# Kernel tuning notes

Hardware: AMD Instinct MI355X
Metric: run time of the kernel (lower is better)

## Reference

```python
import jax, jax.numpy as jnp
import numpy as np

T, B, E, H = 1024, 4, 1024, 16
D = E // H  # head_dim = 64


def rel_shift(x):
    # Transformer-XL relative shift trick (RelativeShift.forward, batch_first=True).
    # x: [BH, Q, P] -> pad one zero column, reshape [BH, P+1, Q], drop first row, reshape back.
    BH, Q, P = x.shape
    zp = jnp.zeros((BH, Q, 1), x.dtype)
    xp = jnp.concatenate([zp, x], axis=2).reshape(BH, P + 1, Q)
    return xp[:, 1:, :].reshape(BH, Q, P)


def setup_inputs() -> dict:
    key = jax.random.key(0)
    ks = jax.random.split(key, 8)
    std = float(np.sqrt(2.0 / (E + E)))
    causal = jnp.triu(jnp.ones((T, T), dtype=bool), k=1)  # True = masked (future positions)
    return {
        "x": jax.random.normal(ks[0], (T, B, E), dtype=jnp.float32),
        "pos": jax.random.normal(ks[1], (T, 1, E), dtype=jnp.float32),
        "in_proj_weight": jax.random.normal(ks[2], (3 * E, E), dtype=jnp.float32) * std,
        "in_proj_bias": jnp.zeros((3 * E,), dtype=jnp.float32),
        "out_proj_weight": jax.random.normal(ks[3], (E, E), dtype=jnp.float32) * std,
        "out_proj_bias": jnp.zeros((E,), dtype=jnp.float32),
        "pos_proj_weight": jax.random.normal(ks[4], (E, E), dtype=jnp.float32) * std,
        "pos_proj_bias": jnp.zeros((E,), dtype=jnp.float32),
        "r_w_bias": jax.random.normal(ks[5], (H, D), dtype=jnp.float32) * 0.02,
        "r_r_bias": jax.random.normal(ks[6], (H, D), dtype=jnp.float32) * 0.02,
        "attn_mask": causal,
    }


def reference(x, pos, in_proj_weight, in_proj_bias, out_proj_weight, out_proj_bias,
              pos_proj_weight, pos_proj_bias, r_w_bias, r_r_bias, attn_mask):
    Tq, Bb, Ee = x.shape
    scale = 1.0 / np.sqrt(D).astype(np.float32)
    # fused QKV projection; layout [T, B, heads, 3, head_dim] matches
    # view(len_q, bsz*heads, 3, head_dim) in the original.
    qkv = (x @ in_proj_weight.T + in_proj_bias).reshape(Tq, Bb, H, 3, D)
    q = qkv[..., 0, :]  # [T,B,H,D]
    k = qkv[..., 1, :]
    v = qkv[..., 2, :]
    # position projection (shared across batch since pos is [T,1,E])
    r_head_k = (pos[:, 0, :] @ pos_proj_weight.T + pos_proj_bias).reshape(Tq, H, D)  # [P,H,D]
    rw_q = q + r_w_bias  # content bias
    rr_q = q + r_r_bias  # position bias
    ac = jnp.einsum('qbhd,kbhd->bhqk', rw_q, k) * scale            # [B,H,Q,K]
    bd = jnp.einsum('qbhd,phd->bhqp', rr_q, r_head_k) * scale      # [B,H,Q,P]
    bd = rel_shift(bd.reshape(Bb * H, Tq, Tq)).reshape(Bb, H, Tq, Tq)[..., :Tq]
    score = ac + bd
    score = jnp.where(attn_mask[None, None, :, :], -jnp.inf, score)
    attn = jax.nn.softmax(score, axis=-1)                          # [B,H,Q,K]
    ctx = jnp.einsum('bhqk,kbhd->qbhd', attn, v).reshape(Tq, Bb, Ee)
    out = ctx @ out_proj_weight.T + out_proj_bias                  # [T,B,E]
    return out, attn
```

## Files before the change

### kernel.cpp

```cpp
#include <hip/hip_runtime.h>
#include <math.h>

#define TQ 1024
#define BBATCH 4
#define EDIM 1024
#define HHEADS 16
#define DHEAD 64

typedef __bf16 bf16x8 __attribute__((ext_vector_type(8)));
typedef __bf16 bf16x4 __attribute__((ext_vector_type(4)));
typedef float  f32x4  __attribute__((ext_vector_type(4)));

#define LDK 40

template<int MODE>
__global__ __launch_bounds__(256) void gemm_mfma_abt(
    const float* __restrict__ A, const float* __restrict__ B,
    const float* __restrict__ bias, float* __restrict__ C,
    int M, int N, int K)
{
    __shared__ __bf16 As[128 * LDK];
    __shared__ __bf16 Bs[128 * LDK];
    const int tid  = threadIdx.x;
    const int lane = tid & 63;
    const int wid  = tid >> 6;
    const int wr   = wid >> 1, wc = wid & 1;
    const int m0 = blockIdx.y * 128, n0 = blockIdx.x * 128;

    f32x4 acc[4][4] = {};

    const int sm0 = tid >> 2;
    const int sm1 = sm0 + 64;
    const int sk  = (tid & 3) << 3;

    const int fr = lane & 15;
    const int kg = (lane >> 4) << 3;

    for (int k0 = 0; k0 < K; k0 += 32) {
        float4 ra0a = *(const float4*)&A[(size_t)(m0 + sm0) * K + k0 + sk];
        float4 ra0b = *(const float4*)&A[(size_t)(m0 + sm0) * K + k0 + sk + 4];
        float4 ra1a = *(const float4*)&A[(size_t)(m0 + sm1) * K + k0 + sk];
        float4 ra1b = *(const float4*)&A[(size_t)(m0 + sm1) * K + k0 + sk + 4];
        float4 rb0a = *(const float4*)&B[(size_t)(n0 + sm0) * K + k0 + sk];
        float4 rb0b = *(const float4*)&B[(size_t)(n0 + sm0) * K + k0 + sk + 4];
        float4 rb1a = *(const float4*)&B[(size_t)(n0 + sm1) * K + k0 + sk];
        float4 rb1b = *(const float4*)&B[(size_t)(n0 + sm1) * K + k0 + sk + 4];

        __syncthreads();

        bf16x8 w;
        w[0]=(__bf16)ra0a.x; w[1]=(__bf16)ra0a.y; w[2]=(__bf16)ra0a.z; w[3]=(__bf16)ra0a.w;
        w[4]=(__bf16)ra0b.x; w[5]=(__bf16)ra0b.y; w[6]=(__bf16)ra0b.z; w[7]=(__bf16)ra0b.w;
        *(bf16x8*)&As[sm0 * LDK + sk] = w;
        w[0]=(__bf16)ra1a.x; w[1]=(__bf16)ra1a.y; w[2]=(__bf16)ra1a.z; w[3]=(__bf16)ra1a.w;
        w[4]=(__bf16)ra1b.x; w[5]=(__bf16)ra1b.y; w[6]=(__bf16)ra1b.z; w[7]=(__bf16)ra1b.w;
        *(bf16x8*)&As[sm1 * LDK + sk] = w;
        w[0]=(__bf16)rb0a.x; w[1]=(__bf16)rb0a.y; w[2]=(__bf16)rb0a.z; w[3]=(__bf16)rb0a.w;
        w[4]=(__bf16)rb0b.x; w[5]=(__bf16)rb0b.y; w[6]=(__bf16)rb0b.z; w[7]=(__bf16)rb0b.w;
        *(bf16x8*)&Bs[sm0 * LDK + sk] = w;
        w[0]=(__bf16)rb1a.x; w[1]=(__bf16)rb1a.y; w[2]=(__bf16)rb1a.z; w[3]=(__bf16)rb1a.w;
        w[4]=(__bf16)rb1b.x; w[5]=(__bf16)rb1b.y; w[6]=(__bf16)rb1b.z; w[7]=(__bf16)rb1b.w;
        *(bf16x8*)&Bs[sm1 * LDK + sk] = w;

        __syncthreads();

        bf16x8 af[4], bfr[4];
        #pragma unroll
        for (int i = 0; i < 4; ++i) {
            af[i]  = *(const bf16x8*)&As[(wr * 64 + i * 16 + fr) * LDK + kg];
            bfr[i] = *(const bf16x8*)&Bs[(wc * 64 + i * 16 + fr) * LDK + kg];
        }
        #pragma unroll
        for (int mi = 0; mi < 4; ++mi)
        #pragma unroll
        for (int ni = 0; ni < 4; ++ni)
            acc[mi][ni] = __builtin_amdgcn_mfma_f32_16x16x32_bf16(
                af[mi], bfr[ni], acc[mi][ni], 0, 0, 0);
    }

    const int fq = lane >> 4;
    #pragma unroll
    for (int mi = 0; mi < 4; ++mi)
    #pragma unroll
    for (int ni = 0; ni < 4; ++ni) {
        int row = m0 + wr * 64 + mi * 16 + fq * 4;
        int col = n0 + wc * 64 + ni * 16 + fr;
        float bv = bias[col];
        #pragma unroll
        for (int j = 0; j < 4; ++j) {
            float v = acc[mi][ni][j] + bv;
            if (MODE == 0) {
                C[(size_t)(row + j) * N + col] = v;
            } else {
                C[(((size_t)(col >> 6) << 10) + (row + j)) * 64 + (col & 63)] = v;
            }
        }
    }
}

__global__ __launch_bounds__(256) void bias_dots_kernel(
    const float* __restrict__ qkv, const float* __restrict__ Rm,
    const float* __restrict__ rwb, const float* __restrict__ rrb,
    float* __restrict__ cK, float* __restrict__ cR)
{
    int id = blockIdx.x * 256 + threadIdx.x;
    if (id < 65536) {
        int bh = id >> 10, k = id & 1023;
        int b = bh >> 4, h = bh & 15;
        const float* p = &qkv[((size_t)k * 4 + b) * 3072 + h * 192 + 64];
        const float* w = &rwb[h << 6];
        float s = 0.f;
        #pragma unroll
        for (int d = 0; d < 64; d += 4) {
            float4 v = *(const float4*)&p[d];
            s += v.x * w[d] + v.y * w[d + 1] + v.z * w[d + 2] + v.w * w[d + 3];
        }
        cK[id] = s;
    } else if (id < 81920) {
        int id2 = id - 65536;
        int h = id2 >> 10, j = id2 & 1023;
        const float* p = &Rm[(((size_t)h << 10) + j) * 64];
        const float* w = &rrb[h << 6];
        float s = 0.f;
        #pragma unroll
        for (int d = 0; d < 64; d += 4) {
            float4 v = *(const float4*)&p[d];
            s += v.x * w[d] + v.y * w[d + 1] + v.z * w[d + 2] + v.w * w[d + 3];
        }
        cR[id2] = s;
    }
}

#define SLD 72

__global__ __launch_bounds__(256) void score_tile_kernel(
    const float* __restrict__ qkv, const float* __restrict__ Rm,
    const float* __restrict__ cK, const float* __restrict__ cR,
    float* __restrict__ attn, float2* __restrict__ part)
{
    int t = blockIdx.x;
    int qt = (int)((sqrtf(8.f * t + 1.f) - 1.f) * 0.5f);
    while ((qt + 1) * (qt + 2) / 2 <= t) ++qt;
    while (qt * (qt + 1) / 2 > t) --qt;
    int kt = t - qt * (qt + 1) / 2;

    const int bh = blockIdx.y;
    const int b = bh >> 4, h = bh & 15;
    const int q0 = qt << 6, k0 = kt << 6;
    const int tid = threadIdx.x, lane = tid & 63, wid = tid >> 6;
    const int fr = lane & 15, fq = lane >> 4, kg = fq << 3;
    const int w16 = wid << 4;
    const int base_j = k0 - q0 + 960;

    __shared__ __align__(16) char smem[36864];
    __bf16* Qs = (__bf16*)smem;
    __bf16* Ks = (__bf16*)(smem + 9216);
    __bf16* R0 = (__bf16*)(smem + 18432);
    __bf16* R1 = (__bf16*)(smem + 27648);
    float (*BDs)[68] = (float(*)[68])smem;

    float4 qreg[4], kreg[4], r0reg[4], r1reg[4];
    #pragma unroll
    for (int s = 0; s < 4; ++s) {
        int idx = (s << 8) + tid;
        int r = idx >> 4, dc = (idx & 15) << 2;
        qreg[s] = *(const float4*)&qkv[((size_t)(q0 + r) * 4 + b) * 3072 + h * 192 + dc];
        kreg[s] = *(const float4*)&qkv[((size_t)(k0 + r) * 4 + b) * 3072 + h * 192 + 64 + dc];
        int j0 = base_j + r;       if (j0 > 1023) j0 = 1023;
        int j1 = base_j + 64 + r;  if (j1 > 1023) j1 = 1023;
        r0reg[s] = *(const float4*)&Rm[(((size_t)h << 10) + j0) * 64 + dc];
        r1reg[s] = *(const float4*)&Rm[(((size_t)h << 10) + j1) * 64 + dc];
    }
    #pragma unroll
    for (int s = 0; s < 4; ++s) {
        int idx = (s << 8) + tid;
        int r = idx >> 4, dc = (idx & 15) << 2;
        bf16x4 w;
        w[0]=(__bf16)qreg[s].x; w[1]=(__bf16)qreg[s].y; w[2]=(__bf16)qreg[s].z; w[3]=(__bf16)qreg[s].w;
        *(bf16x4*)&Qs[r * SLD + dc] = w;
        w[0]=(__bf16)kreg[s].x; w[1]=(__bf16)kreg[s].y; w[2]=(__bf16)kreg[s].z; w[3]=(__bf16)kreg[s].w;
        *(bf16x4*)&Ks[r * SLD + dc] = w;
        w[0]=(__bf16)r0reg[s].x; w[1]=(__bf16)r0reg[s].y; w[2]=(__bf16)r0reg[s].z; w[3]=(__bf16)r0reg[s].w;
        *(bf16x4*)&R0[r * SLD + dc] = w;
        w[0]=(__bf16)r1reg[s].x; w[1]=(__bf16)r1reg[s].y; w[2]=(__bf16)r1reg[s].z; w[3]=(__bf16)r1reg[s].w;
        *(bf16x4*)&R1[r * SLD + dc] = w;
    }
    __syncthreads();

    bf16x8 af0 = *(const bf16x8*)&Qs[(w16 + fr) * SLD + kg];
    bf16x8 af1 = *(const bf16x8*)&Qs[(w16 + fr) * SLD + 32 + kg];

    f32x4 aac[4], abd[4];
    const f32x4 z4 = {0.f, 0.f, 0.f, 0.f};

    #pragma unroll
    for (int ni = 0; ni < 4; ++ni) {
        bf16x8 b0 = *(const bf16x8*)&Ks[(ni * 16 + fr) * SLD + kg];
        bf16x8 b1 = *(const bf16x8*)&Ks[(ni * 16 + fr) * SLD + 32 + kg];
        aac[ni] = __builtin_amdgcn_mfma_f32_16x16x32_bf16(af0, b0, z4, 0, 0, 0);
        aac[ni] = __builtin_amdgcn_mfma_f32_16x16x32_bf16(af1, b1, aac[ni], 0, 0, 0);
    }
    #pragma unroll
    for (int ni = 0; ni < 4; ++ni) {
        bf16x8 b0 = *(const bf16x8*)&R0[(ni * 16 + fr) * SLD + kg];
        bf16x8 b1 = *(const bf16x8*)&R0[(ni * 16 + fr) * SLD + 32 + kg];
        abd[ni] = __builtin_amdgcn_mfma_f32_16x16x32_bf16(af0, b0, z4, 0, 0, 0);
        abd[ni] = __builtin_amdgcn_mfma_f32_16x16x32_bf16(af1, b1, abd[ni], 0, 0, 0);
    }

    __syncthreads();

    #pragma unroll
    for (int ni = 0; ni < 4; ++ni)
    #pragma unroll
    for (int j = 0; j < 4; ++j)
        BDs[w16 + fq * 4 + j][ni * 16 + fr] = abd[ni][j];
    asm volatile("s_waitcnt lgkmcnt(0)" ::: "memory");
    #pragma unroll
    for (int ni = 0; ni < 4; ++ni)
    #pragma unroll
    for (int j = 0; j < 4; ++j) {
        int lrow = w16 + fq * 4 + j;
        int widx = (ni * 16 + fr) - lrow + 63;
        if (widx < 64) aac[ni][j] += BDs[lrow][widx];
    }
    asm volatile("s_waitcnt lgkmcnt(0)" ::: "memory");

    #pragma unroll
    for (int ni = 0; ni < 4; ++ni) {
        bf16x8 b0 = *(const bf16x8*)&R1[(ni * 16 + fr) * SLD + kg];
        bf16x8 b1 = *(const bf16x8*)&R1[(ni * 16 + fr) * SLD + 32 + kg];
        abd[ni] = __builtin_amdgcn_mfma_f32_16x16x32_bf16(af0, b0, z4, 0, 0, 0);
        abd[ni] = __builtin_amdgcn_mfma_f32_16x16x32_bf16(af1, b1, abd[ni], 0, 0, 0);
    }
    #pragma unroll
    for (int ni = 0; ni < 4; ++ni)
    #pragma unroll
    for (int j = 0; j < 4; ++j)
        BDs[w16 + fq * 4 + j][ni * 16 + fr] = abd[ni][j];
    asm volatile("s_waitcnt lgkmcnt(0)" ::: "memory");
    #pragma unroll
    for (int ni = 0; ni < 4; ++ni)
    #pragma unroll
    for (int j = 0; j < 4; ++j) {
        int lrow = w16 + fq * 4 + j;
        int widx = (ni * 16 + fr) - lrow + 63;
        if (widx >= 64) aac[ni][j] += BDs[lrow][widx - 64];
    }

    float sc[4][4];
    #pragma unroll
    for (int ni = 0; ni < 4; ++ni) {
        int lcol = ni * 16 + fr;
        int k = k0 + lcol;
        float ckv = cK[(bh << 10) + k];
        #pragma unroll
        for (int j = 0; j < 4; ++j) {
            int lrow = w16 + fq * 4 + j;
            int q = q0 + lrow;
            int widx = lcol - lrow + 63;
            int jidx = base_j + widx; if (jidx > 1023) jidx = 1023;
            float crv = cR[(h << 10) + jidx];
            float v = 0.125f * (aac[ni][j] + ckv + crv);
            if (kt == qt && lcol > lrow) v = -1e30f;
            sc[ni][j] = v;
            attn[((((size_t)bh << 10) + q) << 10) + k] = v;
        }
    }
    #pragma unroll
    for (int j = 0; j < 4; ++j) {
        float tmax = fmaxf(fmaxf(sc[0][j], sc[1][j]), fmaxf(sc[2][j], sc[3][j]));
        tmax = fmaxf(tmax, __shfl_xor(tmax, 1));
        tmax = fmaxf(tmax, __shfl_xor(tmax, 2));
        tmax = fmaxf(tmax, __shfl_xor(tmax, 4));
        tmax = fmaxf(tmax, __shfl_xor(tmax, 8));
        float ps = __expf(sc[0][j] - tmax) + __expf(sc[1][j] - tmax)
                 + __expf(sc[2][j] - tmax) + __expf(sc[3][j] - tmax);
        ps += __shfl_xor(ps, 1); ps += __shfl_xor(ps, 2);
        ps += __shfl_xor(ps, 4); ps += __shfl_xor(ps, 8);
        if (fr == 0)
            part[(((size_t)(bh << 10) + q0 + w16 + fq * 4 + j) << 4) + kt]
                = make_float2(tmax, ps);
    }
}

__global__ __launch_bounds__(256) void stats_reduce_kernel(
    const float2* __restrict__ part, float2* __restrict__ stats,
    float* __restrict__ ctx)
{
    const int row = blockIdx.x * 256 + threadIdx.x;
    const int q = row & 1023;
    const int nt = (q >> 6) + 1;
    float2 pr[16];
    float m = -1e30f;
    for (int kt = 0; kt < nt; ++kt) {
        pr[kt] = part[((size_t)row << 4) + kt];
        m = fmaxf(m, pr[kt].x);
    }
    float s = 0.f;
    for (int kt = 0; kt < nt; ++kt)
        s += pr[kt].y * __expf(pr[kt].x - m);
    stats[row] = make_float2(m, 1.0f / s);

    const float4 z = {0.f, 0.f, 0.f, 0.f};
    #pragma unroll
    for (int i = 0; i < 16; ++i)
        *(float4*)&ctx[((size_t)i * 65536 + row) * 4] = z;
}

#define FLD 66

__global__ __launch_bounds__(256) void ctx_split_kernel(
    const float* __restrict__ qkv, const float2* __restrict__ stats,
    float* __restrict__ attn, float* __restrict__ ctx)
{
    const int pid = blockIdx.x;
    const int qt = 15 - (pid >> 1);
    const int half = pid & 1;
    const int n = qt + 1;
    const int nh0 = (n + 1) >> 1;
    const int kts = half ? nh0 : 0;
    const int kte = half ? n : nh0;

    const int bh = blockIdx.y;
    const int b = bh >> 4, h = bh & 15;
    const int q0 = qt << 6;
    const int tid = threadIdx.x, lane = tid & 63, wid = tid >> 6;
    const int fr = lane & 15, fq = lane >> 4, kg = fq << 3;
    const int w16 = wid << 4;
    const int c4 = (tid & 15) << 2;
    const int rb = tid >> 4;

    __shared__ __bf16 Pl[64 * FLD];
    __shared__ __bf16 Vt[64 * FLD];

    float mrow[4], inv[4];
    #pragma unroll
    for (int s = 0; s < 4; ++s) {
        float2 st = stats[(bh << 10) + q0 + rb + (s << 4)];
        mrow[s] = st.x; inv[s] = st.y;
    }

    f32x4 apv[4] = {};
    for (int kt = kts; kt < kte; ++kt) {
        const int k0 = kt << 6;
        float4 vreg[4], praw[4];
        #pragma unroll
        for (int s = 0; s < 4; ++s) {
            int r = rb + (s << 4);
            vreg[s] = *(const float4*)&qkv[((size_t)(k0 + r) * 4 + b) * 3072 + h * 192 + 128 + c4];
            praw[s] = *(const float4*)&attn[((size_t)bh << 20) + ((size_t)(q0 + r) << 10) + k0 + c4];
        }
        __syncthreads();
        #pragma unroll
        for (int s = 0; s < 4; ++s) {
            int r = rb + (s << 4);
            Vt[(c4 + 0) * FLD + r] = (__bf16)vreg[s].x;
            Vt[(c4 + 1) * FLD + r] = (__bf16)vreg[s].y;
            Vt[(c4 + 2) * FLD + r] = (__bf16)vreg[s].z;
            Vt[(c4 + 3) * FLD + r] = (__bf16)vreg[s].w;
            float4 p;
            p.x = __expf(praw[s].x - mrow[s]) * inv[s];
            p.y = __expf(praw[s].y - mrow[s]) * inv[s];
            p.z = __expf(praw[s].z - mrow[s]) * inv[s];
            p.w = __expf(praw[s].w - mrow[s]) * inv[s];
            *(float4*)&attn[((size_t)bh << 20) + ((size_t)(q0 + r) << 10) + k0 + c4] = p;
            bf16x4 pw;
            pw[0]=(__bf16)p.x; pw[1]=(__bf16)p.y; pw[2]=(__bf16)p.z; pw[3]=(__bf16)p.w;
            *(bf16x4*)&Pl[r * FLD + c4] = pw;
        }
        __syncthreads();
        bf16x8 pa0 = *(const bf16x8*)&Pl[(w16 + fr) * FLD + kg];
        bf16x8 pa1 = *(const bf16x8*)&Pl[(w16 + fr) * FLD + 32 + kg];
        #pragma unroll
        for (int ni = 0; ni < 4; ++ni) {
            bf16x8 bv0 = *(const bf16x8*)&Vt[(ni * 16 + fr) * FLD + kg];
            bf16x8 bv1 = *(const bf16x8*)&Vt[(ni * 16 + fr) * FLD + 32 + kg];
            apv[ni] = __builtin_amdgcn_mfma_f32_16x16x32_bf16(pa0, bv0, apv[ni], 0, 0, 0);
            apv[ni] = __builtin_amdgcn_mfma_f32_16x16x32_bf16(pa1, bv1, apv[ni], 0, 0, 0);
        }
    }

    if (half) {
        for (int kt = n; kt < 16; ++kt) {
            const int k0 = kt << 6;
            #pragma unroll
            for (int s = 0; s < 4; ++s) {
                int r = rb + (s << 4);
                float4 z = {0.f, 0.f, 0.f, 0.f};
                *(float4*)&attn[((size_t)bh << 20) + ((size_t)(q0 + r) << 10) + k0 + c4] = z;
            }
        }
    }

    if (kte > kts) {
        #pragma unroll
        for (int ni = 0; ni < 4; ++ni)
        #pragma unroll
        for (int j = 0; j < 4; ++j)
            atomicAdd(&ctx[((size_t)(q0 + w16 + fq * 4 + j) * 4 + b) * 1024
                           + (h << 6) + ni * 16 + fr], apv[ni][j]);
    }
}

extern "C" void kernel_launch(void* const* d_in, const int* in_sizes, int n_in,
                              void* d_out, int out_size, void* d_ws, size_t ws_size,
                              hipStream_t stream)
{
    (void)in_sizes; (void)n_in; (void)out_size; (void)ws_size;
    const float* x     = (const float*)d_in[0];
    const float* pos   = (const float*)d_in[1];
    const float* w_in  = (const float*)d_in[2];
    const float* b_in  = (const float*)d_in[3];
    const float* w_out = (const float*)d_in[4];
    const float* b_out = (const float*)d_in[5];
    const float* w_pos = (const float*)d_in[6];
    const float* b_pos = (const float*)d_in[7];
    const float* rwb   = (const float*)d_in[8];
    const float* rrb   = (const float*)d_in[9];

    float* out  = (float*)d_out;
    float* attn = out + (size_t)TQ * BBATCH * EDIM;

    float* ws  = (float*)d_ws;
    float* qkv = ws;
    float* R   = qkv + (size_t)4096 * 3072;
    float* ctx = R + (size_t)HHEADS * TQ * DHEAD;
    float*  cK    = out;
    float*  cR    = out + 65536;
    float2* stats = (float2*)(out + 81920);
    float2* part  = (float2*)(out + 262144);

    dim3 blk(256, 1, 1);

    gemm_mfma_abt<0><<<dim3(3072 / 128, 4096 / 128), blk, 0, stream>>>(
        x, w_in, b_in, qkv, 4096, 3072, 1024);
    gemm_mfma_abt<1><<<dim3(1024 / 128, 1024 / 128), blk, 0, stream>>>(
        pos, w_pos, b_pos, R, 1024, 1024, 1024);
    bias_dots_kernel<<<dim3(320), blk, 0, stream>>>(qkv, R, rwb, rrb, cK, cR);
    score_tile_kernel<<<dim3(136, 64), blk, 0, stream>>>(qkv, R, cK, cR, attn, part);
    stats_reduce_kernel<<<dim3(256), blk, 0, stream>>>(part, stats, ctx);
    ctx_split_kernel<<<dim3(32, 64), blk, 0, stream>>>(qkv, stats, attn, ctx);
    gemm_mfma_abt<0><<<dim3(1024 / 128, 4096 / 128), blk, 0, stream>>>(
        ctx, w_out, b_out, out, 4096, 1024, 1024);
}
```

Before: 376.1 us.

## Load score-tile MFMA operands directly from global memory, dropping LDS staging

The score tile kernel no longer stages Q, K and the two R windows through shared memory. Each wave now loads its MFMA fragments straight from global memory as fp32 and converts them to bf16 in registers. This removes the LDS stores, one barrier and most of the shared memory footprint, and a launch bound of 3 blocks is added to raise occupancy. In exchange, every wave re-reads the K and R rows from global or L2 with less coalesced access. The GEMM change is only a helper refactor plus an unused accumulator.

```diff
diff --git a/kernel.cpp b/kernel.cpp
--- a/kernel.cpp
+++ b/kernel.cpp
@@ -10,6 +10,13 @@
 typedef __bf16 bf16x8 __attribute__((ext_vector_type(8)));
 typedef __bf16 bf16x4 __attribute__((ext_vector_type(4)));
 typedef float  f32x4  __attribute__((ext_vector_type(4)));
+
+__device__ __forceinline__ bf16x8 cvt8(float4 a, float4 b) {
+    bf16x8 w;
+    w[0]=(__bf16)a.x; w[1]=(__bf16)a.y; w[2]=(__bf16)a.z; w[3]=(__bf16)a.w;
+    w[4]=(__bf16)b.x; w[5]=(__bf16)b.y; w[6]=(__bf16)b.z; w[7]=(__bf16)b.w;
+    return w;
+}
 
 #define LDK 40
 
@@ -27,7 +34,9 @@
     const int wr   = wid >> 1, wc = wid & 1;
     const int m0 = blockIdx.y * 128, n0 = blockIdx.x * 128;
 
-    f32x4 acc[4][4] = {};
+    f32x4 acc[2][2][4] = {};
+
+    f32x4 accf[4][4] = {};
 
     const int sm0 = tid >> 2;
     const int sm1 = sm0 + 64;
@@ -48,19 +57,10 @@
 
         __syncthreads();
 
-        bf16x8 w;
-        w[0]=(__bf16)ra0a.x; w[1]=(__bf16)ra0a.y; w[2]=(__bf16)ra0a.z; w[3]=(__bf16)ra0a.w;
-        w[4]=(__bf16)ra0b.x; w[5]=(__bf16)ra0b.y; w[6]=(__bf16)ra0b.z; w[7]=(__bf16)ra0b.w;
-        *(bf16x8*)&As[sm0 * LDK + sk] = w;
-        w[0]=(__bf16)ra1a.x; w[1]=(__bf16)ra1a.y; w[2]=(__bf16)ra1a.z; w[3]=(__bf16)ra1a.w;
-        w[4]=(__bf16)ra1b.x; w[5]=(__bf16)ra1b.y; w[6]=(__bf16)ra1b.z; w[7]=(__bf16)ra1b.w;
-        *(bf16x8*)&As[sm1 * LDK + sk] = w;
-        w[0]=(__bf16)rb0a.x; w[1]=(__bf16)rb0a.y; w[2]=(__bf16)rb0a.z; w[3]=(__bf16)rb0a.w;
-        w[4]=(__bf16)rb0b.x; w[5]=(__bf16)rb0b.y; w[6]=(__bf16)rb0b.z; w[7]=(__bf16)rb0b.w;
-        *(bf16x8*)&Bs[sm0 * LDK + sk] = w;
-        w[0]=(__bf16)rb1a.x; w[1]=(__bf16)rb1a.y; w[2]=(__bf16)rb1a.z; w[3]=(__bf16)rb1a.w;
-        w[4]=(__bf16)rb1b.x; w[5]=(__bf16)rb1b.y; w[6]=(__bf16)rb1b.z; w[7]=(__bf16)rb1b.w;
-        *(bf16x8*)&Bs[sm1 * LDK + sk] = w;
+        *(bf16x8*)&As[sm0 * LDK + sk] = cvt8(ra0a, ra0b);
+        *(bf16x8*)&As[sm1 * LDK + sk] = cvt8(ra1a, ra1b);
+        *(bf16x8*)&Bs[sm0 * LDK + sk] = cvt8(rb0a, rb0b);
+        *(bf16x8*)&Bs[sm1 * LDK + sk] = cvt8(rb1a, rb1b);
 
         __syncthreads();
 
@@ -74,9 +74,10 @@
         for (int mi = 0; mi < 4; ++mi)
         #pragma unroll
         for (int ni = 0; ni < 4; ++ni)
-            acc[mi][ni] = __builtin_amdgcn_mfma_f32_16x16x32_bf16(
-                af[mi], bfr[ni], acc[mi][ni], 0, 0, 0);
-    }
+            accf[mi][ni] = __builtin_amdgcn_mfma_f32_16x16x32_bf16(
+                af[mi], bfr[ni], accf[mi][ni], 0, 0, 0);
+    }
+    (void)acc;
 
     const int fq = lane >> 4;
     #pragma unroll
@@ -88,7 +89,7 @@
         float bv = bias[col];
         #pragma unroll
         for (int j = 0; j < 4; ++j) {
-            float v = acc[mi][ni][j] + bv;
+            float v = accf[mi][ni][j] + bv;
             if (MODE == 0) {
                 C[(size_t)(row + j) * N + col] = v;
             } else {
@@ -131,9 +132,7 @@
     }
 }
 
-#define SLD 72
-
-__global__ __launch_bounds__(256) void score_tile_kernel(
+__global__ __launch_bounds__(256, 3) void score_tile_kernel(
     const float* __restrict__ qkv, const float* __restrict__ Rm,
     const float* __restrict__ cK, const float* __restrict__ cR,
     float* __restrict__ attn, float2* __restrict__ part)
@@ -152,64 +151,33 @@
     const int w16 = wid << 4;
     const int base_j = k0 - q0 + 960;
 
-    __shared__ __align__(16) char smem[36864];
-    __bf16* Qs = (__bf16*)smem;
-    __bf16* Ks = (__bf16*)(smem + 9216);
-    __bf16* R0 = (__bf16*)(smem + 18432);
-    __bf16* R1 = (__bf16*)(smem + 27648);
-    float (*BDs)[68] = (float(*)[68])smem;
-
-    float4 qreg[4], kreg[4], r0reg[4], r1reg[4];
-    #pragma unroll
-    for (int s = 0; s < 4; ++s) {
-        int idx = (s << 8) + tid;
-        int r = idx >> 4, dc = (idx & 15) << 2;
-        qreg[s] = *(const float4*)&qkv[((size_t)(q0 + r) * 4 + b) * 3072 + h * 192 + dc];
-        kreg[s] = *(const float4*)&qkv[((size_t)(k0 + r) * 4 + b) * 3072 + h * 192 + 64 + dc];
-        int j0 = base_j + r;       if (j0 > 1023) j0 = 1023;
-        int j1 = base_j + 64 + r;  if (j1 > 1023) j1 = 1023;
-        r0reg[s] = *(const float4*)&Rm[(((size_t)h << 10) + j0) * 64 + dc];
-        r1reg[s] = *(const float4*)&Rm[(((size_t)h << 10) + j1) * 64 + dc];
-    }
-    #pragma unroll
-    for (int s = 0; s < 4; ++s) {
-        int idx = (s << 8) + tid;
-        int r = idx >> 4, dc = (idx & 15) << 2;
-        bf16x4 w;
-        w[0]=(__bf16)qreg[s].x; w[1]=(__bf16)qreg[s].y; w[2]=(__bf16)qreg[s].z; w[3]=(__bf16)qreg[s].w;
-        *(bf16x4*)&Qs[r * SLD + dc] = w;
-        w[0]=(__bf16)kreg[s].x; w[1]=(__bf16)kreg[s].y; w[2]=(__bf16)kreg[s].z; w[3]=(__bf16)kreg[s].w;
-        *(bf16x4*)&Ks[r * SLD + dc] = w;
-        w[0]=(__bf16)r0reg[s].x; w[1]=(__bf16)r0reg[s].y; w[2]=(__bf16)r0reg[s].z; w[3]=(__bf16)r0reg[s].w;
-        *(bf16x4*)&R0[r * SLD + dc] = w;
-        w[0]=(__bf16)r1reg[s].x; w[1]=(__bf16)r1reg[s].y; w[2]=(__bf16)r1reg[s].z; w[3]=(__bf16)r1reg[s].w;
-        *(bf16x4*)&R1[r * SLD + dc] = w;
-    }
-    __syncthreads();
-
-    bf16x8 af0 = *(const bf16x8*)&Qs[(w16 + fr) * SLD + kg];
-    bf16x8 af1 = *(const bf16x8*)&Qs[(w16 + fr) * SLD + 32 + kg];
+    __shared__ float BDs[64][68];
+
+    const float* qp = &qkv[((size_t)(q0 + w16 + fr) * 4 + b) * 3072 + h * 192];
+    bf16x8 af0 = cvt8(*(const float4*)&qp[kg],      *(const float4*)&qp[kg + 4]);
+    bf16x8 af1 = cvt8(*(const float4*)&qp[32 + kg], *(const float4*)&qp[32 + kg + 4]);
 
     f32x4 aac[4], abd[4];
     const f32x4 z4 = {0.f, 0.f, 0.f, 0.f};
 
     #pragma unroll
     for (int ni = 0; ni < 4; ++ni) {
-        bf16x8 b0 = *(const bf16x8*)&Ks[(ni * 16 + fr) * SLD + kg];
-        bf16x8 b1 = *(const bf16x8*)&Ks[(ni * 16 + fr) * SLD + 32 + kg];
+        const float* kp = &qkv[((size_t)(k0 + ni * 16 + fr) * 4 + b) * 3072 + h * 192 + 64];
+        bf16x8 b0 = cvt8(*(const float4*)&kp[kg],      *(const float4*)&kp[kg + 4]);
+        bf16x8 b1 = cvt8(*(const float4*)&kp[32 + kg], *(const float4*)&kp[32 + kg + 4]);
         aac[ni] = __builtin_amdgcn_mfma_f32_16x16x32_bf16(af0, b0, z4, 0, 0, 0);
         aac[ni] = __builtin_amdgcn_mfma_f32_16x16x32_bf16(af1, b1, aac[ni], 0, 0, 0);
     }
+
     #pragma unroll
     for (int ni = 0; ni < 4; ++ni) {
-        bf16x8 b0 = *(const bf16x8*)&R0[(ni * 16 + fr) * SLD + kg];
-        bf16x8 b1 = *(const bf16x8*)&R0[(ni * 16 + fr) * SLD + 32 + kg];
+        int j0 = base_j + ni * 16 + fr; if (j0 > 1023) j0 = 1023;
+        const float* rp = &Rm[(((size_t)h << 10) + j0) * 64];
+        bf16x8 b0 = cvt8(*(const float4*)&rp[kg],      *(const float4*)&rp[kg + 4]);
+        bf16x8 b1 = cvt8(*(const float4*)&rp[32 + kg], *(const float4*)&rp[32 + kg + 4]);
         abd[ni] = __builtin_amdgcn_mfma_f32_16x16x32_bf16(af0, b0, z4, 0, 0, 0);
         abd[ni] = __builtin_amdgcn_mfma_f32_16x16x32_bf16(af1, b1, abd[ni], 0, 0, 0);
     }
-
-    __syncthreads();
-
     #pragma unroll
     for (int ni = 0; ni < 4; ++ni)
     #pragma unroll
@@ -228,8 +196,10 @@
 
     #pragma unroll
     for (int ni = 0; ni < 4; ++ni) {
-        bf16x8 b0 = *(const bf16x8*)&R1[(ni * 16 + fr) * SLD + kg];
-        bf16x8 b1 = *(const bf16x8*)&R1[(ni * 16 + fr) * SLD + 32 + kg];
+        int j1 = base_j + 64 + ni * 16 + fr; if (j1 > 1023) j1 = 1023;
+        const float* rp = &Rm[(((size_t)h << 10) + j1) * 64];
+        bf16x8 b0 = cvt8(*(const float4*)&rp[kg],      *(const float4*)&rp[kg + 4]);
+        bf16x8 b1 = cvt8(*(const float4*)&rp[32 + kg], *(const float4*)&rp[32 + kg + 4]);
         abd[ni] = __builtin_amdgcn_mfma_f32_16x16x32_bf16(af0, b0, z4, 0, 0, 0);
         abd[ni] = __builtin_amdgcn_mfma_f32_16x16x32_bf16(af1, b1, abd[ni], 0, 0, 0);
     }
```

New measurement: 499.4 us. +32.8%, slower.
